# Optimization experiments

Hardware: AMD Instinct MI355X
Metric: run time of the kernel (lower is better)

Reference implementation:

```python
import jax, jax.numpy as jnp
import numpy as np
from jax.scipy.special import logsumexp

B, L, WLEN = 8, 64, 32
VOCAB, EMB, HID, REC = 30000, 256, 512, 128
PRIOR_FACTOR = 1.0
NEG = -1e9


def setup_inputs():
    key = jax.random.key(0)
    ks = jax.random.split(key, 12)
    h2 = HID // 2
    s = lambda k, shape, sc=0.05: jax.random.normal(k, shape, jnp.float32) * sc
    return {
        "sents": jax.random.randint(ks[0], (B, L, WLEN), 0, VOCAB),
        "mask": jnp.ones((B, L, WLEN), jnp.float32),
        "prior": jax.random.normal(ks[1], (B, L, L), dtype=jnp.float32),
        "heads": jax.random.randint(ks[2], (B, L), 0, L),
        "emb": s(ks[3], (VOCAB, EMB), 0.1),
        "Wih_f": s(ks[4], (4 * h2, EMB)), "Whh_f": s(ks[5], (4 * h2, h2)),
        "bih_f": jnp.zeros((4 * h2,), jnp.float32), "bhh_f": jnp.zeros((4 * h2,), jnp.float32),
        "Wih_b": s(ks[6], (4 * h2, EMB)), "Whh_b": s(ks[7], (4 * h2, h2)),
        "bih_b": jnp.zeros((4 * h2,), jnp.float32), "bhh_b": jnp.zeros((4 * h2,), jnp.float32),
        "W1": s(ks[8], (REC, HID)), "b1": jnp.zeros((REC,), jnp.float32),
        "W2": s(ks[9], (REC, HID)), "b2": jnp.zeros((REC,), jnp.float32),
        "Ws": s(ks[10], (1, 6 * HID)), "bs": jnp.zeros((1,), jnp.float32),
    }


def _lstm_dir(x, Wih, Whh, bih, bhh, reverse):
    # torch nn.LSTM default (no batch_first) scans over dim0; we faithfully scan axis 0.
    Hh = Whh.shape[1]
    bias = bih + bhh

    def step(carry, xt):
        h, c = carry
        g = xt @ Wih.T + h @ Whh.T + bias  # [L, 4H], gate order i,f,g,o
        i, f, gg, o = jnp.split(g, 4, axis=-1)
        c = jax.nn.sigmoid(f) * c + jax.nn.sigmoid(i) * jnp.tanh(gg)
        h = jax.nn.sigmoid(o) * jnp.tanh(c)
        return (h, c), h

    z = jnp.zeros((x.shape[1], Hh), x.dtype)
    _, hs = jax.lax.scan(step, (z, z), x, reverse=reverse)
    return hs


def _eisner_log_partition(s):
    # Eisner inside algorithm (log partition over projective trees rooted at index 0).
    Bz, n = s.shape[0], s.shape[1]
    eye = jnp.eye(n, dtype=s.dtype)
    init = jnp.tile(jnp.where(eye > 0, 0.0, NEG)[None], (Bz, 1, 1))
    C_r, C_l = init, init
    I_r = jnp.full((Bz, n, n), NEG, s.dtype)
    I_l = I_r
    for w in range(1, n):  # static unroll over span widths (sequential DP)
        i = np.arange(n - w)
        j = i + w
        k0 = i[:, None] + np.arange(w)[None, :]         # k = i..j-1
        inc = logsumexp(C_r[:, i[:, None], k0] + C_l[:, k0 + 1, j[:, None]], axis=2)
        I_r = I_r.at[:, i, j].set(inc + s[:, i, j])
        I_l = I_l.at[:, i, j].set(inc + s[:, j, i])
        k1 = i[:, None] + np.arange(1, w + 1)[None, :]  # k = i+1..j
        C_r = C_r.at[:, i, j].set(logsumexp(I_r[:, i[:, None], k1] + C_r[:, k1, j[:, None]], axis=2))
        C_l = C_l.at[:, i, j].set(logsumexp(C_l[:, i[:, None], k0] + I_l[:, k0, j[:, None]], axis=2))
    return C_r[:, 0, n - 1]


def _forward(sents, mask, prior, heads, emb, Wih_f, Whh_f, bih_f, bhh_f,
             Wih_b, Whh_b, bih_b, bhh_b, W1, b1, W2, b2, Ws, bs):
    words = emb[sents]                                   # [B,L,W,E]
    elen = mask.sum(-1)                                  # [B,L]
    embeds = (words * mask[..., None]).sum(2) / (elen + (elen == 0))[..., None]
    h = jnp.concatenate([_lstm_dir(embeds, Wih_f, Whh_f, bih_f, bhh_f, False),
                         _lstm_dir(embeds, Wih_b, Whh_b, bih_b, bhh_b, True)], axis=-1)  # [B,L,HID]
    xn = jnp.pad(h[:, 1:], ((0, 0), (0, 1), (0, 0)))     # next-EDU shift
    xb = jnp.pad(h[:, :-1], ((0, 0), (1, 0), (0, 0)))    # prev-EDU shift
    trio = jnp.concatenate([h, xb, xn], axis=-1)         # [B,L,3*HID]
    Bz, n, F3 = trio.shape
    # pairwise feature tensor (materialized as in the original module)
    f = jnp.concatenate([jnp.broadcast_to(trio[:, :, None, :], (Bz, n, n, F3)),
                         jnp.broadcast_to(trio[:, None, :, :], (Bz, n, n, F3))], axis=-1)
    crf = jnp.einsum('bijk,k->bij', f, Ws[0]) + bs[0]    # [B,n,n]
    p1 = h @ W1.T + b1
    p2 = h @ W2.T + b2
    recons = jax.nn.log_softmax(jnp.einsum('bik,bjk->bij', p1, p2), axis=-1)
    jp = crf + recons + (PRIOR_FACTOR / n) * prior
    logZ = _eisner_log_partition(crf)                    # [B]
    g = jp[jnp.arange(Bz)[:, None], heads[:, 1:], jnp.arange(1, n)[None, :]]  # [B,n-1]
    best = logsumexp(g, axis=1)
    return -(best - logZ).mean()


def reference(sents, mask, prior, heads, emb, Wih_f, Whh_f, bih_f, bhh_f,
              Wih_b, Whh_b, bih_b, bhh_b, W1, b1, W2, b2, Ws, bs):
    return _forward(sents, mask, prior, heads, emb, Wih_f, Whh_f, bih_f, bhh_f,
                    Wih_b, Whh_b, bih_b, bhh_b, W1, b1, W2, b2, Ws, bs)
```

## Files before the change

### kernel.cpp

```cpp
#include <hip/hip_runtime.h>
#include <hip/hip_bf16.h>
#include <math.h>

#define L2E 1.44269504f
#define LN2 0.69314718f
#define TSTRIDE 68

typedef __attribute__((ext_vector_type(2))) float floatx2;

__device__ __forceinline__ float sigf(float x){ return 1.0f/(1.0f+expf(-x)); }

__device__ __forceinline__ float quad_max(float x) {
    x = fmaxf(x, __int_as_float(__builtin_amdgcn_mov_dpp(__float_as_int(x), 0xB1, 0xF, 0xF, true)));
    x = fmaxf(x, __int_as_float(__builtin_amdgcn_mov_dpp(__float_as_int(x), 0x4E, 0xF, 0xF, true)));
    return x;
}
__device__ __forceinline__ float oct_sum(float x) {
    x += __int_as_float(__builtin_amdgcn_mov_dpp(__float_as_int(x), 0xB1, 0xF, 0xF, true));
    x += __int_as_float(__builtin_amdgcn_mov_dpp(__float_as_int(x), 0x4E, 0xF, 0xF, true));
    x += __int_as_float(__builtin_amdgcn_mov_dpp(__float_as_int(x), 0x141, 0xF, 0xF, true));
    return x;
}

__global__ __launch_bounds__(256) void prep_all(const float* __restrict__ Whh_f, const float* __restrict__ Whh_b,
                             const float* __restrict__ bih_f, const float* __restrict__ bhh_f,
                             const float* __restrict__ bih_b, const float* __restrict__ bhh_b,
                             uint4* __restrict__ qWf, uint4* __restrict__ qWb,
                             float* __restrict__ scf, float* __restrict__ scb,
                             float* __restrict__ biasf, float* __restrict__ biasb,
                             const int* __restrict__ sents, const float* __restrict__ mask,
                             const float* __restrict__ emb, float* __restrict__ embeds,
                             float* __restrict__ out) {
    int tid = threadIdx.x;
    if (blockIdx.x < 512) {
        int bl = blockIdx.x;
        const int*   srow = sents + bl*32;
        const float* mrow = mask  + bl*32;
        float acc = 0.0f, el = 0.0f;
        for (int w = 0; w < 32; ++w) {
            float m = mrow[w];
            el  += m;
            acc += emb[(size_t)srow[w]*256 + tid] * m;
        }
        float den = el + (el == 0.0f ? 1.0f : 0.0f);
        embeds[bl*256 + tid] = acc / den;
        if (bl == 0)      { for (int q = tid; q < 1024; q += 256) biasf[q] = bih_f[q] + bhh_f[q]; }
        else if (bl == 1) { for (int q = tid; q < 1024; q += 256) biasb[q] = bih_b[q] + bhh_b[q]; }
        else if (bl == 2 && tid == 0) out[0] = 0.0f;
    } else {
        int pb  = blockIdx.x - 512;
        int dir = pb >> 6;
        int cg  = pb & 63;
        const float* W = dir ? Whh_b : Whh_f;
        uint4* qW = dir ? qWb : qWf;
        float* sc = dir ? scb : scf;
        __shared__ float Wl[16][260];
        __shared__ float sL[16];
        #pragma unroll
        for (int lr = 0; lr < 16; ++lr) {
            int g = lr >> 2, jj = lr & 3;
            int rowid = g*256 + cg*4 + jj;
            Wl[lr][tid] = W[(size_t)rowid*256 + tid];
        }
        __syncthreads();
        if (tid < 64) {
            int lr = tid >> 2, sub = tid & 3;
            float mx = 0.0f;
            for (int m = 0; m < 64; ++m) mx = fmaxf(mx, fabsf(Wl[lr][sub*64 + m]));
            mx = quad_max(mx);
            if (sub == 0) sL[lr] = mx * (1.0f/240.0f) + 1e-30f;
        }
        __syncthreads();
        int k4 = tid >> 2, jj = tid & 3;
        float is0 = 1.0f / sL[0*4 + jj];
        float is1 = 1.0f / sL[1*4 + jj];
        float is2 = 1.0f / sL[2*4 + jj];
        float is3 = 1.0f / sL[3*4 + jj];
        uint4 q;
        unsigned int* qq = (unsigned int*)&q;
        #pragma unroll
        for (int kk = 0; kk < 4; ++kk) {
            int k = k4*4 + kk;
            int d = 0;
            d = __builtin_amdgcn_cvt_pk_fp8_f32(Wl[0*4+jj][k]*is0, Wl[1*4+jj][k]*is1, d, false);
            d = __builtin_amdgcn_cvt_pk_fp8_f32(Wl[2*4+jj][k]*is2, Wl[3*4+jj][k]*is3, d, true);
            qq[kk] = (unsigned int)d;
        }
        qW[k4*256 + cg*4 + jj] = q;
        if (tid < 16) {
            int g = tid >> 2, j2 = tid & 3;
            sc[(cg*4 + j2)*4 + g] = sL[g*4 + j2];
        }
    }
}

__device__ __forceinline__ void gemm64_body(const float* __restrict__ A,
                                            const float* __restrict__ Bm,
                                            const float* __restrict__ bias,
                                            float* __restrict__ C,
                                            int N, int K, int bx, int by) {
    __shared__ __align__(16) float As[32][68];
    __shared__ __align__(16) float Bs[32][68];
    int tid = threadIdx.x;
    int tx = tid & 15, ty = tid >> 4;
    int row0 = bx * 64, col0 = by * 64;
    float acc[4][4];
    #pragma unroll
    for (int r = 0; r < 4; ++r)
        #pragma unroll
        for (int c = 0; c < 4; ++c) acc[r][c] = 0.0f;
    int lr = tid >> 2;
    int lc = (tid & 3) * 8;
    for (int k0 = 0; k0 < K; k0 += 32) {
        float4 a0 = *(const float4*)(A  + (size_t)(row0+lr)*K + k0 + lc);
        float4 a1 = *(const float4*)(A  + (size_t)(row0+lr)*K + k0 + lc + 4);
        float4 b0 = *(const float4*)(Bm + (size_t)(col0+lr)*K + k0 + lc);
        float4 b1 = *(const float4*)(Bm + (size_t)(col0+lr)*K + k0 + lc + 4);
        As[lc  ][lr] = a0.x; As[lc+1][lr] = a0.y; As[lc+2][lr] = a0.z; As[lc+3][lr] = a0.w;
        As[lc+4][lr] = a1.x; As[lc+5][lr] = a1.y; As[lc+6][lr] = a1.z; As[lc+7][lr] = a1.w;
        Bs[lc  ][lr] = b0.x; Bs[lc+1][lr] = b0.y; Bs[lc+2][lr] = b0.z; Bs[lc+3][lr] = b0.w;
        Bs[lc+4][lr] = b1.x; Bs[lc+5][lr] = b1.y; Bs[lc+6][lr] = b1.z; Bs[lc+7][lr] = b1.w;
        __syncthreads();
        #pragma unroll
        for (int kc = 0; kc < 32; ++kc) {
            float4 xa = *(const float4*)&As[kc][ty*4];
            float4 xb = *(const float4*)&Bs[kc][tx*4];
            acc[0][0] = fmaf(xa.x, xb.x, acc[0][0]);
            acc[0][1] = fmaf(xa.x, xb.y, acc[0][1]);
            acc[0][2] = fmaf(xa.x, xb.z, acc[0][2]);
            acc[0][3] = fmaf(xa.x, xb.w, acc[0][3]);
            acc[1][0] = fmaf(xa.y, xb.x, acc[1][0]);
            acc[1][1] = fmaf(xa.y, xb.y, acc[1][1]);
            acc[1][2] = fmaf(xa.y, xb.z, acc[1][2]);
            acc[1][3] = fmaf(xa.y, xb.w, acc[1][3]);
            acc[2][0] = fmaf(xa.z, xb.x, acc[2][0]);
            acc[2][1] = fmaf(xa.z, xb.y, acc[2][1]);
            acc[2][2] = fmaf(xa.z, xb.z, acc[2][2]);
            acc[2][3] = fmaf(xa.z, xb.w, acc[2][3]);
            acc[3][0] = fmaf(xa.w, xb.x, acc[3][0]);
            acc[3][1] = fmaf(xa.w, xb.y, acc[3][1]);
            acc[3][2] = fmaf(xa.w, xb.z, acc[3][2]);
            acc[3][3] = fmaf(xa.w, xb.w, acc[3][3]);
        }
        __syncthreads();
    }
    float4 bv = bias ? *(const float4*)&bias[col0 + tx*4] : make_float4(0.f,0.f,0.f,0.f);
    #pragma unroll
    for (int r = 0; r < 4; ++r) {
        float4 o;
        o.x = acc[r][0] + bv.x; o.y = acc[r][1] + bv.y;
        o.z = acc[r][2] + bv.z; o.w = acc[r][3] + bv.w;
        *(float4*)(C + (size_t)(row0 + ty*4 + r)*N + col0 + tx*4) = o;
    }
}

__device__ __forceinline__ void gemm32_body(const float* __restrict__ A,
                                            const float* __restrict__ Bm,
                                            const float* __restrict__ bias,
                                            float* __restrict__ C,
                                            int N, int K, int bx, int by) {
    __shared__ __align__(16) float As[32][36];
    __shared__ __align__(16) float Bs[32][36];
    int tid = threadIdx.x;
    int tx = tid & 15, ty = tid >> 4;
    int row0 = bx * 32, col0 = by * 32;
    float acc00 = 0.f, acc01 = 0.f, acc10 = 0.f, acc11 = 0.f;
    int lr = tid >> 3;
    int lc = (tid & 7) * 4;
    for (int k0 = 0; k0 < K; k0 += 32) {
        float4 a0 = *(const float4*)(A  + (size_t)(row0+lr)*K + k0 + lc);
        float4 b0 = *(const float4*)(Bm + (size_t)(col0+lr)*K + k0 + lc);
        As[lc  ][lr] = a0.x; As[lc+1][lr] = a0.y; As[lc+2][lr] = a0.z; As[lc+3][lr] = a0.w;
        Bs[lc  ][lr] = b0.x; Bs[lc+1][lr] = b0.y; Bs[lc+2][lr] = b0.z; Bs[lc+3][lr] = b0.w;
        __syncthreads();
        #pragma unroll
        for (int kc = 0; kc < 32; ++kc) {
            float2 xa = *(const float2*)&As[kc][ty*2];
            float2 xb = *(const float2*)&Bs[kc][tx*2];
            acc00 = fmaf(xa.x, xb.x, acc00);
            acc01 = fmaf(xa.x, xb.y, acc01);
            acc10 = fmaf(xa.y, xb.x, acc10);
            acc11 = fmaf(xa.y, xb.y, acc11);
        }
        __syncthreads();
    }
    float2 bv = *(const float2*)&bias[col0 + tx*2];
    float2 o0; o0.x = acc00 + bv.x; o0.y = acc01 + bv.y;
    float2 o1; o1.x = acc10 + bv.x; o1.y = acc11 + bv.y;
    *(float2*)(C + (size_t)(row0 + ty*2    )*N + col0 + tx*2) = o0;
    *(float2*)(C + (size_t)(row0 + ty*2 + 1)*N + col0 + tx*2) = o1;
}

__global__ __launch_bounds__(256) void gemm_ih(const float* __restrict__ embeds,
                                               const float* __restrict__ Wf, const float* __restrict__ Wb,
                                               const float* __restrict__ biasf, const float* __restrict__ biasb,
                                               float* __restrict__ gxf, float* __restrict__ gxb) {
    int dir = blockIdx.z;
    gemm64_body(embeds, dir ? Wb : Wf, dir ? biasb : biasf, dir ? gxb : gxf,
                1024, 256, blockIdx.x, blockIdx.y);
}

__global__ __launch_bounds__(512) void lstm_rec(const float* __restrict__ gxf,
                                                const float* __restrict__ gxb,
                                                const uint4* __restrict__ qWf,
                                                const uint4* __restrict__ qWb,
                                                const float* __restrict__ scf,
                                                const float* __restrict__ scb,
                                                float* __restrict__ hall) {
    int blk  = blockIdx.x;
    int rep  = blk >> 7;
    blk &= 127;
    int dir  = blk >> 6;
    int pos  = blk & 63;
    int tid  = threadIdx.x;
    int j    = tid & 255;
    int half = tid >> 8;
    const float* gx = dir ? gxb : gxf;
    const uint4* qW = dir ? qWb : qWf;
    float4 sc = ((const float4*)(dir ? scb : scf))[j];
    __shared__ __align__(16) float hs[256];
    __shared__ __align__(16) float part[256][4];
    if (tid < 256) hs[tid] = 0.0f;
    float cellc = 0.0f;
    __syncthreads();
    const uint4* qWh = qW + (half << 13);
    const float* hsh = hs + (half << 7);
    for (int s = 0; s < 8; ++s) {
        int t = dir ? (7 - s) : s;
        const float* g0 = gx + (size_t)(t*64 + pos)*1024;
        float ai = 0.0f, af = 0.0f, ag = 0.0f, ao = 0.0f;
        if (half == 0) { ai = g0[j]; af = g0[256+j]; ag = g0[512+j]; ao = g0[768+j]; }
        float qi = 0.0f, qf = 0.0f, qg = 0.0f, qo = 0.0f;
        #pragma unroll 8
        for (int k4 = 0; k4 < 32; ++k4) {
            uint4 wq = qWh[(k4 << 8) + j];
            float4 hp = *(const float4*)&hsh[k4*4];
            floatx2 pa, pb;
            pa = __builtin_amdgcn_cvt_pk_f32_fp8(wq.x, false);
            pb = __builtin_amdgcn_cvt_pk_f32_fp8(wq.x, true);
            qi = fmaf(pa.x, hp.x, qi); qf = fmaf(pa.y, hp.x, qf);
            qg = fmaf(pb.x, hp.x, qg); qo = fmaf(pb.y, hp.x, qo);
            pa = __builtin_amdgcn_cvt_pk_f32_fp8(wq.y, false);
            pb = __builtin_amdgcn_cvt_pk_f32_fp8(wq.y, true);
            qi = fmaf(pa.x, hp.y, qi); qf = fmaf(pa.y, hp.y, qf);
            qg = fmaf(pb.x, hp.y, qg); qo = fmaf(pb.y, hp.y, qo);
            pa = __builtin_amdgcn_cvt_pk_f32_fp8(wq.z, false);
            pb = __builtin_amdgcn_cvt_pk_f32_fp8(wq.z, true);
            qi = fmaf(pa.x, hp.z, qi); qf = fmaf(pa.y, hp.z, qf);
            qg = fmaf(pb.x, hp.z, qg); qo = fmaf(pb.y, hp.z, qo);
            pa = __builtin_amdgcn_cvt_pk_f32_fp8(wq.w, false);
            pb = __builtin_amdgcn_cvt_pk_f32_fp8(wq.w, true);
            qi = fmaf(pa.x, hp.w, qi); qf = fmaf(pa.y, hp.w, qf);
            qg = fmaf(pb.x, hp.w, qg); qo = fmaf(pb.y, hp.w, qo);
        }
        if (half) { part[j][0] = qi; part[j][1] = qf; part[j][2] = qg; part[j][3] = qo; }
        __syncthreads();
        if (half == 0) {
            float4 pr = *(const float4*)&part[j][0];
            ai = fmaf(sc.x, qi + pr.x, ai);
            af = fmaf(sc.y, qf + pr.y, af);
            ag = fmaf(sc.z, qg + pr.z, ag);
            ao = fmaf(sc.w, qo + pr.w, ao);
            cellc = sigf(af)*cellc + sigf(ai)*tanhf(ag);
            float h0 = sigf(ao)*tanhf(cellc);
            hs[j] = h0;
            if (rep == 0) hall[(size_t)(t*64 + pos)*512 + dir*256 + j] = h0;
        }
        __syncthreads();
    }
}

__global__ __launch_bounds__(256) void post_lstm(const float* __restrict__ hall,
                                                 const float* __restrict__ Ws,
                                                 float* __restrict__ u, float* __restrict__ v,
                                                 const float* __restrict__ W1, const float* __restrict__ b1,
                                                 const float* __restrict__ W2, const float* __restrict__ b2,
                                                 float* __restrict__ p1, float* __restrict__ p2) {
    if (blockIdx.x < 512) {
        int bi = blockIdx.x;
        int i  = bi & 63;
        int tid = threadIdx.x;
        float pu = 0.0f, pv = 0.0f;
        for (int q = tid; q < 1536; q += 256) {
            int seg = q >> 9, kk = q & 511;
            float tv = 0.0f;
            if (seg == 0)       tv = hall[(size_t)bi*512 + kk];
            else if (seg == 1)  { if (i > 0)  tv = hall[(size_t)(bi-1)*512 + kk]; }
            else                { if (i < 63) tv = hall[(size_t)(bi+1)*512 + kk]; }
            pu = fmaf(tv, Ws[q],        pu);
            pv = fmaf(tv, Ws[1536 + q], pv);
        }
        for (int off = 32; off; off >>= 1) { pu += __shfl_xor(pu, off); pv += __shfl_xor(pv, off); }
        __shared__ float ru[4], rv[4];
        int wv = tid >> 6, lane = tid & 63;
        if (lane == 0) { ru[wv] = pu; rv[wv] = pv; }
        __syncthreads();
        if (tid == 0) { u[bi] = ru[0]+ru[1]+ru[2]+ru[3]; v[bi] = rv[0]+rv[1]+rv[2]+rv[3]; }
    } else {
        int gb = blockIdx.x - 512;
        int sel = gb >> 6; gb &= 63;
        gemm32_body(hall, sel ? W2 : W1, sel ? b2 : b1, sel ? p2 : p1,
                    128, 512, gb >> 2, gb & 3);
    }
}

__global__ __launch_bounds__(512, 2) void eisner_final(const float* __restrict__ u,
                                                    const float* __restrict__ v,
                                                    const float* __restrict__ bs,
                                                    const float* __restrict__ p1,
                                                    const float* __restrict__ p2,
                                                    const float* __restrict__ prior,
                                                    const int* __restrict__ heads,
                                                    float* __restrict__ out) {
    int b   = blockIdx.x & 7;
    int rep = blockIdx.x >> 3;
    __shared__ __align__(16) float SMEM[3*64*TSTRIDE + 64];
    __shared__ float su[64], sv[64], lseSb[64], sBest[1];
    float* T1 = &SMEM[0];
    float* T2 = &SMEM[64*TSTRIDE];
    float* T3 = &SMEM[2*64*TSTRIDE];
    int tid = threadIdx.x;
    float bsv = bs[0];
    if (tid < 64) {
        su[tid] = u[b*64 + tid];
        sv[tid] = v[b*64 + tid];
    }
    const float4* g1 = (const float4*)(p1 + (size_t)b*8192);
    const float4* g2 = (const float4*)(p2 + (size_t)b*8192);
    float4* s1p = (float4*)SMEM;
    float4* s2p = (float4*)(SMEM + 64*TSTRIDE);
    int r   = tid >> 3;
    int sub = tid & 7;
    float acc[8];
    #pragma unroll
    for (int q = 0; q < 8; ++q) acc[q] = 0.0f;
    for (int p = 0; p < 2; ++p) {
        #pragma unroll
        for (int f0 = 0; f0 < 4; ++f0) {
            int f = f0*512 + tid;
            int half = f >> 10;
            int ff = f & 1023;
            int row = ff >> 4, c4 = ff & 15;
            float4 vv = (half ? g2 : g1)[row*32 + (p<<4) + c4];
            (half ? s2p : s1p)[row*17 + c4] = vv;
        }
        __syncthreads();
        #pragma unroll 2
        for (int k4 = 0; k4 < 16; ++k4) {
            float4 a = s1p[r*17 + k4];
            #pragma unroll
            for (int q = 0; q < 8; ++q) {
                float4 bv = s2p[(sub + (q<<3))*17 + k4];
                acc[q] = fmaf(a.x, bv.x, acc[q]);
                acc[q] = fmaf(a.y, bv.y, acc[q]);
                acc[q] = fmaf(a.z, bv.z, acc[q]);
                acc[q] = fmaf(a.w, bv.w, acc[q]);
            }
        }
        __syncthreads();
    }
    float pm = acc[0];
    #pragma unroll
    for (int q = 1; q < 8; ++q) pm = fmaxf(pm, acc[q]);
    pm = fmaxf(pm, __int_as_float(__builtin_amdgcn_mov_dpp(__float_as_int(pm), 0xB1, 0xF, 0xF, true)));
    pm = fmaxf(pm, __int_as_float(__builtin_amdgcn_mov_dpp(__float_as_int(pm), 0x4E, 0xF, 0xF, true)));
    pm = fmaxf(pm, __int_as_float(__builtin_amdgcn_mov_dpp(__float_as_int(pm), 0x141, 0xF, 0xF, true)));
    float ps = 0.0f;
    #pragma unroll
    for (int q = 0; q < 8; ++q) ps += exp2f((acc[q] - pm) * L2E);
    ps = oct_sum(ps);
    if (sub == 0) lseSb[r] = pm + log2f(ps) * LN2;
    float* Sl = SMEM;
    #pragma unroll
    for (int q = 0; q < 8; ++q) Sl[r*66 + sub + (q<<3)] = acc[q];
    __syncthreads();
    if (tid < 64) {
        int m = tid;
        float gv = -INFINITY;
        if (m >= 1) {
            int hd = heads[b*64 + m];
            gv = su[hd] + sv[m] + bsv + (Sl[hd*66 + m] - lseSb[hd])
               + prior[(size_t)(b*64 + hd)*64 + m] * (1.0f/64.0f);
        }
        float mm = gv;
        for (int off = 32; off; off >>= 1) mm = fmaxf(mm, __shfl_xor(mm, off));
        float se = (m >= 1) ? exp2f((gv - mm) * L2E) : 0.0f;
        for (int off = 32; off; off >>= 1) se += __shfl_xor(se, off);
        if (m == 0) sBest[0] = mm + log2f(se) * LN2;
    }
    __syncthreads();
    for (int q = tid; q < 3*64*TSTRIDE; q += 512) SMEM[q] = 0.0f;
    __syncthreads();
    if (tid < 64) {
        T1[tid*TSTRIDE + tid] = 1.0f;
        if (tid >= 1) T2[tid*TSTRIDE + tid-1] = 1.0f;
    }
    __syncthreads();
    int i = r;
    int k0 = i & ~3;
    float sui_b = su[i] + bsv;
    float svi_b = sv[i] + bsv;
    const float* t1i = &T1[i*TSTRIDE];
    const float* t2i = &T2[i*TSTRIDE];
    const float* t3i = &T3[i*TSTRIDE];
    for (int w = 1; w < 64; ++w) {
        int ns = 64 - w;
        if (i < ns) {
            int j = i + w;
            const float* t1j = &T1[j*TSTRIDE];
            const float* t2j = &T2[j*TSTRIDE];
            const float* t3j = &T3[j*TSTRIDE];
            float eDr = exp2f((sui_b + sv[j]) * L2E);
            float eDl = exp2f((su[j] + svi_b) * L2E);
            float s1 = 0.0f, sr = 0.0f, sl = 0.0f;
            #pragma unroll
            for (int t = 0; t < 2; ++t) {
                int k = k0 + ((t << 3) + sub) * 4;
                if (k < j) {
                    float4 a1  = *(const float4*)&t1i[k];
                    float4 b1  = *(const float4*)&t2j[k];
                    float4 a2  = *(const float4*)&t3i[k];
                    float4 b2v = *(const float4*)&t1j[k];
                    float4 a3  = *(const float4*)&t2i[k];
                    float4 b3  = *(const float4*)&t3j[k];
                    #pragma unroll
                    for (int c = 0; c < 4; ++c) {
                        s1 = fmaf(((const float*)&a1)[c], ((const float*)&b1)[c],  s1);
                        sr = fmaf(((const float*)&a2)[c], ((const float*)&b2v)[c], sr);
                        sl = fmaf(((const float*)&a3)[c], ((const float*)&b3)[c],  sl);
                    }
                }
            }
            s1 = oct_sum(s1);
            sr = oct_sum(sr);
            sl = oct_sum(sl);
            if (sub == 0) {
                float Ir = 0.25f * s1 * eDr;
                float Il = 0.25f * s1 * eDl;
                float Cr = sr + Ir;
                float Cl = sl + Il;
                T3[i*TSTRIDE + j] = Ir;
                T1[i*TSTRIDE + j] = Cr;
                T1[j*TSTRIDE + i] = Cr;
                T3[j*TSTRIDE + i] = Il;
                T2[i*TSTRIDE + j] = Cl;
                if (i >= 1) T2[j*TSTRIDE + i-1] = Cl;
            }
        }
        __syncthreads();
    }
    if (rep == 0 && tid == 0) {
        float logZv = (log2f(T1[0*TSTRIDE + 63]) + 126.0f) * LN2;
        atomicAdd(out, -(sBest[0] - logZv) * 0.125f);
    }
}

extern "C" void kernel_launch(void* const* d_in, const int* in_sizes, int n_in,
                              void* d_out, int out_size, void* d_ws, size_t ws_size,
                              hipStream_t stream) {
    const int*   sents = (const int*)  d_in[0];
    const float* mask  = (const float*)d_in[1];
    const float* prior = (const float*)d_in[2];
    const int*   heads = (const int*)  d_in[3];
    const float* emb   = (const float*)d_in[4];
    const float* Wih_f = (const float*)d_in[5];
    const float* Whh_f = (const float*)d_in[6];
    const float* bih_f = (const float*)d_in[7];
    const float* bhh_f = (const float*)d_in[8];
    const float* Wih_b = (const float*)d_in[9];
    const float* Whh_b = (const float*)d_in[10];
    const float* bih_b = (const float*)d_in[11];
    const float* bhh_b = (const float*)d_in[12];
    const float* W1    = (const float*)d_in[13];
    const float* b1    = (const float*)d_in[14];
    const float* W2    = (const float*)d_in[15];
    const float* b2    = (const float*)d_in[16];
    const float* Ws    = (const float*)d_in[17];
    const float* bs    = (const float*)d_in[18];
    float* out = (float*)d_out;

    char* w = (char*)d_ws;
    float* embeds = (float*)(w + 0);
    float* gxf    = (float*)(w + 524288);
    float* gxb    = (float*)(w + 2621440);
    uint4* qWf    = (uint4*)(w + 4718592);
    uint4* qWb    = (uint4*)(w + 4980736);
    float* scf    = (float*)(w + 5242880);
    float* scb    = (float*)(w + 5246976);
    float* biasf  = (float*)(w + 5767168);
    float* biasb  = (float*)(w + 5771264);
    float* hall   = (float*)(w + 5775360);
    float* uArr   = (float*)(w + 6823936);
    float* vArr   = (float*)(w + 6825984);
    float* p1     = (float*)(w + 6828032);
    float* p2     = (float*)(w + 7090176);

    prep_all<<<640, 256, 0, stream>>>(Whh_f, Whh_b, bih_f, bhh_f, bih_b, bhh_b,
                                      qWf, qWb, scf, scb, biasf, biasb,
                                      sents, mask, emb, embeds, out);
    gemm_ih<<<dim3(8,16,2), 256, 0, stream>>>(embeds, Wih_f, Wih_b, biasf, biasb, gxf, gxb);
    lstm_rec<<<256, 512, 0, stream>>>(gxf, gxb, qWf, qWb, scf, scb, hall);
    post_lstm<<<640, 256, 0, stream>>>(hall, Ws, uArr, vArr, W1, b1, W2, b2, p1, p2);
    eisner_final<<<256, 512, 0, stream>>>(uArr, vArr, bs, p1, p2, prior, heads, out);
    (void)in_sizes; (void)n_in; (void)out_size; (void)ws_size;
}
```

Before: 208.9 us.

## Fuse GEMM, LSTM, post-LSTM and Eisner stages into one persistent kernel with grid barriers

Merges the four kernels that ran after prep (input GEMM, LSTM recurrence, post-LSTM projections, Eisner DP) into one persistent kernel of 256 blocks. The stages are separated by a software grid barrier built on an atomic counter, which prep_all resets. The aim is to remove kernel launch gaps and tail effects between stages. The risks are deadlock if all 256 blocks of 512 threads are not co-resident, plus atomic spin overhead, and several stages now have their work split differently across blocks.

```diff
diff --git a/kernel.cpp b/kernel.cpp
--- a/kernel.cpp
+++ b/kernel.cpp
@@ -13,6 +13,12 @@
 __device__ __forceinline__ float quad_max(float x) {
     x = fmaxf(x, __int_as_float(__builtin_amdgcn_mov_dpp(__float_as_int(x), 0xB1, 0xF, 0xF, true)));
     x = fmaxf(x, __int_as_float(__builtin_amdgcn_mov_dpp(__float_as_int(x), 0x4E, 0xF, 0xF, true)));
+    return x;
+}
+__device__ __forceinline__ float oct_max(float x) {
+    x = fmaxf(x, __int_as_float(__builtin_amdgcn_mov_dpp(__float_as_int(x), 0xB1, 0xF, 0xF, true)));
+    x = fmaxf(x, __int_as_float(__builtin_amdgcn_mov_dpp(__float_as_int(x), 0x4E, 0xF, 0xF, true)));
+    x = fmaxf(x, __int_as_float(__builtin_amdgcn_mov_dpp(__float_as_int(x), 0x141, 0xF, 0xF, true)));
     return x;
 }
 __device__ __forceinline__ float oct_sum(float x) {
@@ -20,6 +26,17 @@
     x += __int_as_float(__builtin_amdgcn_mov_dpp(__float_as_int(x), 0x4E, 0xF, 0xF, true));
     x += __int_as_float(__builtin_amdgcn_mov_dpp(__float_as_int(x), 0x141, 0xF, 0xF, true));
     return x;
+}
+
+__device__ __forceinline__ void gbar(unsigned* cnt, unsigned target) {
+    __threadfence();
+    __syncthreads();
+    if (threadIdx.x == 0) {
+        atomicAdd(cnt, 1u);
+        while (atomicAdd(cnt, 0u) < target) __builtin_amdgcn_s_sleep(10);
+    }
+    __syncthreads();
+    __threadfence();
 }
 
 __global__ __launch_bounds__(256) void prep_all(const float* __restrict__ Whh_f, const float* __restrict__ Whh_b,
@@ -30,7 +47,7 @@
                              float* __restrict__ biasf, float* __restrict__ biasb,
                              const int* __restrict__ sents, const float* __restrict__ mask,
                              const float* __restrict__ emb, float* __restrict__ embeds,
-                             float* __restrict__ out) {
+                             float* __restrict__ out, unsigned* __restrict__ bar) {
     int tid = threadIdx.x;
     if (blockIdx.x < 512) {
         int bl = blockIdx.x;
@@ -46,7 +63,7 @@
         embeds[bl*256 + tid] = acc / den;
         if (bl == 0)      { for (int q = tid; q < 1024; q += 256) biasf[q] = bih_f[q] + bhh_f[q]; }
         else if (bl == 1) { for (int q = tid; q < 1024; q += 256) biasb[q] = bih_b[q] + bhh_b[q]; }
-        else if (bl == 2 && tid == 0) out[0] = 0.0f;
+        else if (bl == 2 && tid == 0) { out[0] = 0.0f; atomicExch(bar, 0u); }
     } else {
         int pb  = blockIdx.x - 512;
         int dir = pb >> 6;
@@ -94,364 +111,357 @@
     }
 }
 
-__device__ __forceinline__ void gemm64_body(const float* __restrict__ A,
-                                            const float* __restrict__ Bm,
-                                            const float* __restrict__ bias,
-                                            float* __restrict__ C,
-                                            int N, int K, int bx, int by) {
-    __shared__ __align__(16) float As[32][68];
-    __shared__ __align__(16) float Bs[32][68];
-    int tid = threadIdx.x;
-    int tx = tid & 15, ty = tid >> 4;
-    int row0 = bx * 64, col0 = by * 64;
-    float acc[4][4];
-    #pragma unroll
-    for (int r = 0; r < 4; ++r)
-        #pragma unroll
-        for (int c = 0; c < 4; ++c) acc[r][c] = 0.0f;
-    int lr = tid >> 2;
-    int lc = (tid & 3) * 8;
-    for (int k0 = 0; k0 < K; k0 += 32) {
-        float4 a0 = *(const float4*)(A  + (size_t)(row0+lr)*K + k0 + lc);
-        float4 a1 = *(const float4*)(A  + (size_t)(row0+lr)*K + k0 + lc + 4);
-        float4 b0 = *(const float4*)(Bm + (size_t)(col0+lr)*K + k0 + lc);
-        float4 b1 = *(const float4*)(Bm + (size_t)(col0+lr)*K + k0 + lc + 4);
-        As[lc  ][lr] = a0.x; As[lc+1][lr] = a0.y; As[lc+2][lr] = a0.z; As[lc+3][lr] = a0.w;
-        As[lc+4][lr] = a1.x; As[lc+5][lr] = a1.y; As[lc+6][lr] = a1.z; As[lc+7][lr] = a1.w;
-        Bs[lc  ][lr] = b0.x; Bs[lc+1][lr] = b0.y; Bs[lc+2][lr] = b0.z; Bs[lc+3][lr] = b0.w;
-        Bs[lc+4][lr] = b1.x; Bs[lc+5][lr] = b1.y; Bs[lc+6][lr] = b1.z; Bs[lc+7][lr] = b1.w;
-        __syncthreads();
-        #pragma unroll
-        for (int kc = 0; kc < 32; ++kc) {
-            float4 xa = *(const float4*)&As[kc][ty*4];
-            float4 xb = *(const float4*)&Bs[kc][tx*4];
-            acc[0][0] = fmaf(xa.x, xb.x, acc[0][0]);
-            acc[0][1] = fmaf(xa.x, xb.y, acc[0][1]);
-            acc[0][2] = fmaf(xa.x, xb.z, acc[0][2]);
-            acc[0][3] = fmaf(xa.x, xb.w, acc[0][3]);
-            acc[1][0] = fmaf(xa.y, xb.x, acc[1][0]);
-            acc[1][1] = fmaf(xa.y, xb.y, acc[1][1]);
-            acc[1][2] = fmaf(xa.y, xb.z, acc[1][2]);
-            acc[1][3] = fmaf(xa.y, xb.w, acc[1][3]);
-            acc[2][0] = fmaf(xa.z, xb.x, acc[2][0]);
-            acc[2][1] = fmaf(xa.z, xb.y, acc[2][1]);
-            acc[2][2] = fmaf(xa.z, xb.z, acc[2][2]);
-            acc[2][3] = fmaf(xa.z, xb.w, acc[2][3]);
-            acc[3][0] = fmaf(xa.w, xb.x, acc[3][0]);
-            acc[3][1] = fmaf(xa.w, xb.y, acc[3][1]);
-            acc[3][2] = fmaf(xa.w, xb.z, acc[3][2]);
-            acc[3][3] = fmaf(xa.w, xb.w, acc[3][3]);
-        }
-        __syncthreads();
-    }
-    float4 bv = bias ? *(const float4*)&bias[col0 + tx*4] : make_float4(0.f,0.f,0.f,0.f);
-    #pragma unroll
-    for (int r = 0; r < 4; ++r) {
-        float4 o;
-        o.x = acc[r][0] + bv.x; o.y = acc[r][1] + bv.y;
-        o.z = acc[r][2] + bv.z; o.w = acc[r][3] + bv.w;
-        *(float4*)(C + (size_t)(row0 + ty*4 + r)*N + col0 + tx*4) = o;
-    }
-}
-
-__device__ __forceinline__ void gemm32_body(const float* __restrict__ A,
-                                            const float* __restrict__ Bm,
-                                            const float* __restrict__ bias,
-                                            float* __restrict__ C,
-                                            int N, int K, int bx, int by) {
-    __shared__ __align__(16) float As[32][36];
-    __shared__ __align__(16) float Bs[32][36];
-    int tid = threadIdx.x;
-    int tx = tid & 15, ty = tid >> 4;
-    int row0 = bx * 32, col0 = by * 32;
-    float acc00 = 0.f, acc01 = 0.f, acc10 = 0.f, acc11 = 0.f;
-    int lr = tid >> 3;
-    int lc = (tid & 7) * 4;
-    for (int k0 = 0; k0 < K; k0 += 32) {
-        float4 a0 = *(const float4*)(A  + (size_t)(row0+lr)*K + k0 + lc);
-        float4 b0 = *(const float4*)(Bm + (size_t)(col0+lr)*K + k0 + lc);
-        As[lc  ][lr] = a0.x; As[lc+1][lr] = a0.y; As[lc+2][lr] = a0.z; As[lc+3][lr] = a0.w;
-        Bs[lc  ][lr] = b0.x; Bs[lc+1][lr] = b0.y; Bs[lc+2][lr] = b0.z; Bs[lc+3][lr] = b0.w;
-        __syncthreads();
-        #pragma unroll
-        for (int kc = 0; kc < 32; ++kc) {
-            float2 xa = *(const float2*)&As[kc][ty*2];
-            float2 xb = *(const float2*)&Bs[kc][tx*2];
-            acc00 = fmaf(xa.x, xb.x, acc00);
-            acc01 = fmaf(xa.x, xb.y, acc01);
-            acc10 = fmaf(xa.y, xb.x, acc10);
-            acc11 = fmaf(xa.y, xb.y, acc11);
-        }
-        __syncthreads();
-    }
-    float2 bv = *(const float2*)&bias[col0 + tx*2];
-    float2 o0; o0.x = acc00 + bv.x; o0.y = acc01 + bv.y;
-    float2 o1; o1.x = acc10 + bv.x; o1.y = acc11 + bv.y;
-    *(float2*)(C + (size_t)(row0 + ty*2    )*N + col0 + tx*2) = o0;
-    *(float2*)(C + (size_t)(row0 + ty*2 + 1)*N + col0 + tx*2) = o1;
-}
-
-__global__ __launch_bounds__(256) void gemm_ih(const float* __restrict__ embeds,
-                                               const float* __restrict__ Wf, const float* __restrict__ Wb,
-                                               const float* __restrict__ biasf, const float* __restrict__ biasb,
-                                               float* __restrict__ gxf, float* __restrict__ gxb) {
-    int dir = blockIdx.z;
-    gemm64_body(embeds, dir ? Wb : Wf, dir ? biasb : biasf, dir ? gxb : gxf,
-                1024, 256, blockIdx.x, blockIdx.y);
-}
-
-__global__ __launch_bounds__(512) void lstm_rec(const float* __restrict__ gxf,
-                                                const float* __restrict__ gxb,
-                                                const uint4* __restrict__ qWf,
-                                                const uint4* __restrict__ qWb,
-                                                const float* __restrict__ scf,
-                                                const float* __restrict__ scb,
-                                                float* __restrict__ hall) {
-    int blk  = blockIdx.x;
-    int rep  = blk >> 7;
-    blk &= 127;
-    int dir  = blk >> 6;
-    int pos  = blk & 63;
-    int tid  = threadIdx.x;
-    int j    = tid & 255;
-    int half = tid >> 8;
-    const float* gx = dir ? gxb : gxf;
-    const uint4* qW = dir ? qWb : qWf;
-    float4 sc = ((const float4*)(dir ? scb : scf))[j];
-    __shared__ __align__(16) float hs[256];
-    __shared__ __align__(16) float part[256][4];
-    if (tid < 256) hs[tid] = 0.0f;
-    float cellc = 0.0f;
-    __syncthreads();
-    const uint4* qWh = qW + (half << 13);
-    const float* hsh = hs + (half << 7);
-    for (int s = 0; s < 8; ++s) {
-        int t = dir ? (7 - s) : s;
-        const float* g0 = gx + (size_t)(t*64 + pos)*1024;
-        float ai = 0.0f, af = 0.0f, ag = 0.0f, ao = 0.0f;
-        if (half == 0) { ai = g0[j]; af = g0[256+j]; ag = g0[512+j]; ao = g0[768+j]; }
-        float qi = 0.0f, qf = 0.0f, qg = 0.0f, qo = 0.0f;
-        #pragma unroll 8
-        for (int k4 = 0; k4 < 32; ++k4) {
-            uint4 wq = qWh[(k4 << 8) + j];
-            float4 hp = *(const float4*)&hsh[k4*4];
-            floatx2 pa, pb;
-            pa = __builtin_amdgcn_cvt_pk_f32_fp8(wq.x, false);
-            pb = __builtin_amdgcn_cvt_pk_f32_fp8(wq.x, true);
-            qi = fmaf(pa.x, hp.x, qi); qf = fmaf(pa.y, hp.x, qf);
-            qg = fmaf(pb.x, hp.x, qg); qo = fmaf(pb.y, hp.x, qo);
-            pa = __builtin_amdgcn_cvt_pk_f32_fp8(wq.y, false);
-            pb = __builtin_amdgcn_cvt_pk_f32_fp8(wq.y, true);
-            qi = fmaf(pa.x, hp.y, qi); qf = fmaf(pa.y, hp.y, qf);
-            qg = fmaf(pb.x, hp.y, qg); qo = fmaf(pb.y, hp.y, qo);
-            pa = __builtin_amdgcn_cvt_pk_f32_fp8(wq.z, false);
-            pb = __builtin_amdgcn_cvt_pk_f32_fp8(wq.z, true);
-            qi = fmaf(pa.x, hp.z, qi); qf = fmaf(pa.y, hp.z, qf);
-            qg = fmaf(pb.x, hp.z, qg); qo = fmaf(pb.y, hp.z, qo);
-            pa = __builtin_amdgcn_cvt_pk_f32_fp8(wq.w, false);
-            pb = __builtin_amdgcn_cvt_pk_f32_fp8(wq.w, true);
-            qi = fmaf(pa.x, hp.w, qi); qf = fmaf(pa.y, hp.w, qf);
-            qg = fmaf(pb.x, hp.w, qg); qo = fmaf(pb.y, hp.w, qo);
-        }
-        if (half) { part[j][0] = qi; part[j][1] = qf; part[j][2] = qg; part[j][3] = qo; }
-        __syncthreads();
-        if (half == 0) {
-            float4 pr = *(const float4*)&part[j][0];
-            ai = fmaf(sc.x, qi + pr.x, ai);
-            af = fmaf(sc.y, qf + pr.y, af);
-            ag = fmaf(sc.z, qg + pr.z, ag);
-            ao = fmaf(sc.w, qo + pr.w, ao);
-            cellc = sigf(af)*cellc + sigf(ai)*tanhf(ag);
-            float h0 = sigf(ao)*tanhf(cellc);
-            hs[j] = h0;
-            if (rep == 0) hall[(size_t)(t*64 + pos)*512 + dir*256 + j] = h0;
-        }
-        __syncthreads();
-    }
-}
-
-__global__ __launch_bounds__(256) void post_lstm(const float* __restrict__ hall,
-                                                 const float* __restrict__ Ws,
-                                                 float* __restrict__ u, float* __restrict__ v,
-                                                 const float* __restrict__ W1, const float* __restrict__ b1,
-                                                 const float* __restrict__ W2, const float* __restrict__ b2,
-                                                 float* __restrict__ p1, float* __restrict__ p2) {
-    if (blockIdx.x < 512) {
-        int bi = blockIdx.x;
-        int i  = bi & 63;
-        int tid = threadIdx.x;
-        float pu = 0.0f, pv = 0.0f;
-        for (int q = tid; q < 1536; q += 256) {
-            int seg = q >> 9, kk = q & 511;
-            float tv = 0.0f;
-            if (seg == 0)       tv = hall[(size_t)bi*512 + kk];
-            else if (seg == 1)  { if (i > 0)  tv = hall[(size_t)(bi-1)*512 + kk]; }
-            else                { if (i < 63) tv = hall[(size_t)(bi+1)*512 + kk]; }
-            pu = fmaf(tv, Ws[q],        pu);
-            pv = fmaf(tv, Ws[1536 + q], pv);
-        }
-        for (int off = 32; off; off >>= 1) { pu += __shfl_xor(pu, off); pv += __shfl_xor(pv, off); }
-        __shared__ float ru[4], rv[4];
-        int wv = tid >> 6, lane = tid & 63;
-        if (lane == 0) { ru[wv] = pu; rv[wv] = pv; }
-        __syncthreads();
-        if (tid == 0) { u[bi] = ru[0]+ru[1]+ru[2]+ru[3]; v[bi] = rv[0]+rv[1]+rv[2]+rv[3]; }
-    } else {
-        int gb = blockIdx.x - 512;
-        int sel = gb >> 6; gb &= 63;
-        gemm32_body(hall, sel ? W2 : W1, sel ? b2 : b1, sel ? p2 : p1,
-                    128, 512, gb >> 2, gb & 3);
-    }
-}
-
-__global__ __launch_bounds__(512, 2) void eisner_final(const float* __restrict__ u,
-                                                    const float* __restrict__ v,
-                                                    const float* __restrict__ bs,
-                                                    const float* __restrict__ p1,
-                                                    const float* __restrict__ p2,
-                                                    const float* __restrict__ prior,
-                                                    const int* __restrict__ heads,
-                                                    float* __restrict__ out) {
-    int b   = blockIdx.x & 7;
-    int rep = blockIdx.x >> 3;
+__global__ __launch_bounds__(512, 2) void fused_main(
+        const float* __restrict__ embeds,
+        const float* __restrict__ Wih_f, const float* __restrict__ Wih_b,
+        const float* __restrict__ biasf, const float* __restrict__ biasb,
+        float* __restrict__ gxf, float* __restrict__ gxb,
+        const uint4* __restrict__ qWf, const uint4* __restrict__ qWb,
+        const float* __restrict__ scf, const float* __restrict__ scb,
+        float* __restrict__ hall,
+        const float* __restrict__ Ws, float* __restrict__ u, float* __restrict__ v,
+        const float* __restrict__ W1, const float* __restrict__ b1,
+        const float* __restrict__ W2, const float* __restrict__ b2,
+        float* __restrict__ p1, float* __restrict__ p2,
+        const float* __restrict__ bs, const float* __restrict__ prior,
+        const int* __restrict__ heads,
+        float* __restrict__ out, unsigned* __restrict__ bar) {
     __shared__ __align__(16) float SMEM[3*64*TSTRIDE + 64];
     __shared__ float su[64], sv[64], lseSb[64], sBest[1];
-    float* T1 = &SMEM[0];
-    float* T2 = &SMEM[64*TSTRIDE];
-    float* T3 = &SMEM[2*64*TSTRIDE];
+    __shared__ float ru2[2][4], rv2[2][4];
     int tid = threadIdx.x;
-    float bsv = bs[0];
-    if (tid < 64) {
-        su[tid] = u[b*64 + tid];
-        sv[tid] = v[b*64 + tid];
+    int blk = blockIdx.x;
+
+    {
+        int dir  = blk >> 7;
+        int rest = blk & 127;
+        int bx = rest >> 4, by = rest & 15;
+        const float* A    = embeds;
+        const float* Bm   = dir ? Wih_b : Wih_f;
+        const float* bias = dir ? biasb : biasf;
+        float* C          = dir ? gxb : gxf;
+        const int N = 1024, K = 256;
+        float* As = SMEM;
+        float* Bs = SMEM + 32*68;
+        int tx = tid & 15, ty = tid >> 4;
+        int row0 = bx * 64, col0 = by * 64;
+        float acc[2][4];
+        #pragma unroll
+        for (int r = 0; r < 2; ++r)
+            #pragma unroll
+            for (int c = 0; c < 4; ++c) acc[r][c] = 0.0f;
+        int lr = tid >> 3;
+        int lc = (tid & 7) * 4;
+        for (int k0 = 0; k0 < K; k0 += 32) {
+            float4 a0 = *(const float4*)(A  + (size_t)(row0+lr)*K + k0 + lc);
+            float4 b0 = *(const float4*)(Bm + (size_t)(col0+lr)*K + k0 + lc);
+            As[(lc  )*68 + lr] = a0.x; As[(lc+1)*68 + lr] = a0.y;
+            As[(lc+2)*68 + lr] = a0.z; As[(lc+3)*68 + lr] = a0.w;
+            Bs[(lc  )*68 + lr] = b0.x; Bs[(lc+1)*68 + lr] = b0.y;
+            Bs[(lc+2)*68 + lr] = b0.z; Bs[(lc+3)*68 + lr] = b0.w;
+            __syncthreads();
+            #pragma unroll
+            for (int kc = 0; kc < 32; ++kc) {
+                float2 xa = *(const float2*)&As[kc*68 + ty*2];
+                float4 xb = *(const float4*)&Bs[kc*68 + tx*4];
+                acc[0][0] = fmaf(xa.x, xb.x, acc[0][0]);
+                acc[0][1] = fmaf(xa.x, xb.y, acc[0][1]);
+                acc[0][2] = fmaf(xa.x, xb.z, acc[0][2]);
+                acc[0][3] = fmaf(xa.x, xb.w, acc[0][3]);
+                acc[1][0] = fmaf(xa.y, xb.x, acc[1][0]);
+                acc[1][1] = fmaf(xa.y, xb.y, acc[1][1]);
+                acc[1][2] = fmaf(xa.y, xb.z, acc[1][2]);
+                acc[1][3] = fmaf(xa.y, xb.w, acc[1][3]);
+            }
+            __syncthreads();
+        }
+        float4 bv = *(const float4*)&bias[col0 + tx*4];
+        #pragma unroll
+        for (int r = 0; r < 2; ++r) {
+            float4 o;
+            o.x = acc[r][0] + bv.x; o.y = acc[r][1] + bv.y;
+            o.z = acc[r][2] + bv.z; o.w = acc[r][3] + bv.w;
+            *(float4*)(C + (size_t)(row0 + ty*2 + r)*N + col0 + tx*4) = o;
+        }
     }
-    const float4* g1 = (const float4*)(p1 + (size_t)b*8192);
-    const float4* g2 = (const float4*)(p2 + (size_t)b*8192);
-    float4* s1p = (float4*)SMEM;
-    float4* s2p = (float4*)(SMEM + 64*TSTRIDE);
-    int r   = tid >> 3;
-    int sub = tid & 7;
-    float acc[8];
-    #pragma unroll
-    for (int q = 0; q < 8; ++q) acc[q] = 0.0f;
-    for (int p = 0; p < 2; ++p) {
-        #pragma unroll
-        for (int f0 = 0; f0 < 4; ++f0) {
-            int f = f0*512 + tid;
-            int half = f >> 10;
-            int ff = f & 1023;
-            int row = ff >> 4, c4 = ff & 15;
-            float4 vv = (half ? g2 : g1)[row*32 + (p<<4) + c4];
-            (half ? s2p : s1p)[row*17 + c4] = vv;
-        }
-        __syncthreads();
-        #pragma unroll 2
-        for (int k4 = 0; k4 < 16; ++k4) {
-            float4 a = s1p[r*17 + k4];
+    gbar(bar, 256);
+
+    {
+        int lb   = blk;
+        int rep  = lb >> 7;
+        lb &= 127;
+        int dir  = lb >> 6;
+        int pos  = lb & 63;
+        int j    = tid & 255;
+        int half = tid >> 8;
+        const float* gx = dir ? gxb : gxf;
+        const uint4* qW = dir ? qWb : qWf;
+        float4 sc = ((const float4*)(dir ? scb : scf))[j];
+        float* hs = SMEM;
+        float (*part)[4] = (float(*)[4])(SMEM + 256);
+        if (tid < 256) hs[tid] = 0.0f;
+        float cellc = 0.0f;
+        __syncthreads();
+        const uint4* qWh = qW + (half << 13);
+        const float* hsh = hs + (half << 7);
+        for (int s = 0; s < 8; ++s) {
+            int t = dir ? (7 - s) : s;
+            const float* g0 = gx + (size_t)(t*64 + pos)*1024;
+            float ai = 0.0f, af = 0.0f, ag = 0.0f, ao = 0.0f;
+            if (half == 0) { ai = g0[j]; af = g0[256+j]; ag = g0[512+j]; ao = g0[768+j]; }
+            float qi = 0.0f, qf = 0.0f, qg = 0.0f, qo = 0.0f;
+            #pragma unroll 8
+            for (int k4 = 0; k4 < 32; ++k4) {
+                uint4 wq = qWh[(k4 << 8) + j];
+                float4 hp = *(const float4*)&hsh[k4*4];
+                floatx2 pa, pb;
+                pa = __builtin_amdgcn_cvt_pk_f32_fp8(wq.x, false);
+                pb = __builtin_amdgcn_cvt_pk_f32_fp8(wq.x, true);
+                qi = fmaf(pa.x, hp.x, qi); qf = fmaf(pa.y, hp.x, qf);
+                qg = fmaf(pb.x, hp.x, qg); qo = fmaf(pb.y, hp.x, qo);
+                pa = __builtin_amdgcn_cvt_pk_f32_fp8(wq.y, false);
+                pb = __builtin_amdgcn_cvt_pk_f32_fp8(wq.y, true);
+                qi = fmaf(pa.x, hp.y, qi); qf = fmaf(pa.y, hp.y, qf);
+                qg = fmaf(pb.x, hp.y, qg); qo = fmaf(pb.y, hp.y, qo);
+                pa = __builtin_amdgcn_cvt_pk_f32_fp8(wq.z, false);
+                pb = __builtin_amdgcn_cvt_pk_f32_fp8(wq.z, true);
+                qi = fmaf(pa.x, hp.z, qi); qf = fmaf(pa.y, hp.z, qf);
+                qg = fmaf(pb.x, hp.z, qg); qo = fmaf(pb.y, hp.z, qo);
+                pa = __builtin_amdgcn_cvt_pk_f32_fp8(wq.w, false);
+                pb = __builtin_amdgcn_cvt_pk_f32_fp8(wq.w, true);
+                qi = fmaf(pa.x, hp.w, qi); qf = fmaf(pa.y, hp.w, qf);
+                qg = fmaf(pb.x, hp.w, qg); qo = fmaf(pb.y, hp.w, qo);
+            }
+            if (half) { part[j][0] = qi; part[j][1] = qf; part[j][2] = qg; part[j][3] = qo; }
+            __syncthreads();
+            if (half == 0) {
+                float4 pr = *(const float4*)&part[j][0];
+                ai = fmaf(sc.x, qi + pr.x, ai);
+                af = fmaf(sc.y, qf + pr.y, af);
+                ag = fmaf(sc.z, qg + pr.z, ag);
+                ao = fmaf(sc.w, qo + pr.w, ao);
+                cellc = sigf(af)*cellc + sigf(ai)*tanhf(ag);
+                float h0 = sigf(ao)*tanhf(cellc);
+                hs[j] = h0;
+                if (rep == 0) hall[(size_t)(t*64 + pos)*512 + dir*256 + j] = h0;
+            }
+            __syncthreads();
+        }
+    }
+    gbar(bar, 512);
+
+    if (blk >= 128) {
+        int h  = tid >> 8;
+        int t2 = tid & 255;
+        for (int p = 0; p < 2; ++p) {
+            int bi = (blk - 128)*4 + p*2 + h;
+            int i  = bi & 63;
+            float pu = 0.0f, pv = 0.0f;
+            for (int q = t2; q < 1536; q += 256) {
+                int seg = q >> 9, kk = q & 511;
+                float tv = 0.0f;
+                if (seg == 0)       tv = hall[(size_t)bi*512 + kk];
+                else if (seg == 1)  { if (i > 0)  tv = hall[(size_t)(bi-1)*512 + kk]; }
+                else                { if (i < 63) tv = hall[(size_t)(bi+1)*512 + kk]; }
+                pu = fmaf(tv, Ws[q],        pu);
+                pv = fmaf(tv, Ws[1536 + q], pv);
+            }
+            for (int off = 32; off; off >>= 1) { pu += __shfl_xor(pu, off); pv += __shfl_xor(pv, off); }
+            int wv = t2 >> 6, lane = t2 & 63;
+            if (lane == 0) { ru2[h][wv] = pu; rv2[h][wv] = pv; }
+            __syncthreads();
+            if (t2 == 0) {
+                u[bi] = ru2[h][0]+ru2[h][1]+ru2[h][2]+ru2[h][3];
+                v[bi] = rv2[h][0]+rv2[h][1]+rv2[h][2]+rv2[h][3];
+            }
+            __syncthreads();
+        }
+    } else {
+        int sel = blk >> 6, un = blk & 63;
+        const float* A    = hall;
+        const float* Bm   = sel ? W2 : W1;
+        const float* bias = sel ? b2 : b1;
+        float* C          = sel ? p2 : p1;
+        int bx = un >> 2, by = un & 3;
+        const int N = 128, K = 512;
+        float* As2 = SMEM;
+        float* Bs2 = SMEM + 32*36;
+        int tx = tid & 15, ty = (tid >> 4) & 15;
+        int row0 = bx * 32, col0 = by * 32;
+        float a00 = 0.f, a01 = 0.f, a10 = 0.f, a11 = 0.f;
+        int lr = (tid >> 3) & 31;
+        int lc = (tid & 7) * 4;
+        for (int k0 = 0; k0 < K; k0 += 32) {
+            if (tid < 256) {
+                float4 av = *(const float4*)(A  + (size_t)(row0+lr)*K + k0 + lc);
+                float4 bv = *(const float4*)(Bm + (size_t)(col0+lr)*K + k0 + lc);
+                As2[(lc  )*36 + lr] = av.x; As2[(lc+1)*36 + lr] = av.y;
+                As2[(lc+2)*36 + lr] = av.z; As2[(lc+3)*36 + lr] = av.w;
+                Bs2[(lc  )*36 + lr] = bv.x; Bs2[(lc+1)*36 + lr] = bv.y;
+                Bs2[(lc+2)*36 + lr] = bv.z; Bs2[(lc+3)*36 + lr] = bv.w;
+            }
+            __syncthreads();
+            if (tid < 256) {
+                #pragma unroll
+                for (int kc = 0; kc < 32; ++kc) {
+                    float2 xa = *(const float2*)&As2[kc*36 + ty*2];
+                    float2 xb = *(const float2*)&Bs2[kc*36 + tx*2];
+                    a00 = fmaf(xa.x, xb.x, a00);
+                    a01 = fmaf(xa.x, xb.y, a01);
+                    a10 = fmaf(xa.y, xb.x, a10);
+                    a11 = fmaf(xa.y, xb.y, a11);
+                }
+            }
+            __syncthreads();
+        }
+        if (tid < 256) {
+            float2 bv = *(const float2*)&bias[col0 + tx*2];
+            float2 o0; o0.x = a00 + bv.x; o0.y = a01 + bv.y;
+            float2 o1; o1.x = a10 + bv.x; o1.y = a11 + bv.y;
+            *(float2*)(C + (size_t)(row0 + ty*2    )*N + col0 + tx*2) = o0;
+            *(float2*)(C + (size_t)(row0 + ty*2 + 1)*N + col0 + tx*2) = o1;
+        }
+    }
+    gbar(bar, 768);
+
+    {
+        int b   = blk & 7;
+        int rep = blk >> 3;
+        float* T1 = &SMEM[0];
+        float* T2 = &SMEM[64*TSTRIDE];
+        float* T3 = &SMEM[2*64*TSTRIDE];
+        float bsv = bs[0];
+        if (tid < 64) {
+            su[tid] = u[b*64 + tid];
+            sv[tid] = v[b*64 + tid];
+        }
+        const float4* g1 = (const float4*)(p1 + (size_t)b*8192);
+        const float4* g2 = (const float4*)(p2 + (size_t)b*8192);
+        float4* s1p = (float4*)SMEM;
+        float4* s2p = (float4*)(SMEM + 64*TSTRIDE);
+        int r   = tid >> 3;
+        int sub = tid & 7;
+        float acc[8];
+        #pragma unroll
+        for (int q = 0; q < 8; ++q) acc[q] = 0.0f;
+        __syncthreads();
+        for (int p = 0; p < 2; ++p) {
             #pragma unroll
-            for (int q = 0; q < 8; ++q) {
-                float4 bv = s2p[(sub + (q<<3))*17 + k4];
-                acc[q] = fmaf(a.x, bv.x, acc[q]);
-                acc[q] = fmaf(a.y, bv.y, acc[q]);
-                acc[q] = fmaf(a.z, bv.z, acc[q]);
-                acc[q] = fmaf(a.w, bv.w, acc[q]);
-            }
-        }
-        __syncthreads();
-    }
-    float pm = acc[0];
-    #pragma unroll
-    for (int q = 1; q < 8; ++q) pm = fmaxf(pm, acc[q]);
-    pm = fmaxf(pm, __int_as_float(__builtin_amdgcn_mov_dpp(__float_as_int(pm), 0xB1, 0xF, 0xF, true)));
-    pm = fmaxf(pm, __int_as_float(__builtin_amdgcn_mov_dpp(__float_as_int(pm), 0x4E, 0xF, 0xF, true)));
-    pm = fmaxf(pm, __int_as_float(__builtin_amdgcn_mov_dpp(__float_as_int(pm), 0x141, 0xF, 0xF, true)));
-    float ps = 0.0f;
-    #pragma unroll
-    for (int q = 0; q < 8; ++q) ps += exp2f((acc[q] - pm) * L2E);
-    ps = oct_sum(ps);
-    if (sub == 0) lseSb[r] = pm + log2f(ps) * LN2;
-    float* Sl = SMEM;
-    #pragma unroll
-    for (int q = 0; q < 8; ++q) Sl[r*66 + sub + (q<<3)] = acc[q];
-    __syncthreads();
-    if (tid < 64) {
-        int m = tid;
-        float gv = -INFINITY;
-        if (m >= 1) {
-            int hd = heads[b*64 + m];
-            gv = su[hd] + sv[m] + bsv + (Sl[hd*66 + m] - lseSb[hd])
-               + prior[(size_t)(b*64 + hd)*64 + m] * (1.0f/64.0f);
-        }
-        float mm = gv;
-        for (int off = 32; off; off >>= 1) mm = fmaxf(mm, __shfl_xor(mm, off));
-        float se = (m >= 1) ? exp2f((gv - mm) * L2E) : 0.0f;
-        for (int off = 32; off; off >>= 1) se += __shfl_xor(se, off);
-        if (m == 0) sBest[0] = mm + log2f(se) * LN2;
-    }
-    __syncthreads();
-    for (int q = tid; q < 3*64*TSTRIDE; q += 512) SMEM[q] = 0.0f;
-    __syncthreads();
-    if (tid < 64) {
-        T1[tid*TSTRIDE + tid] = 1.0f;
-        if (tid >= 1) T2[tid*TSTRIDE + tid-1] = 1.0f;
-    }
-    __syncthreads();
-    int i = r;
-    int k0 = i & ~3;
-    float sui_b = su[i] + bsv;
-    float svi_b = sv[i] + bsv;
-    const float* t1i = &T1[i*TSTRIDE];
-    const float* t2i = &T2[i*TSTRIDE];
-    const float* t3i = &T3[i*TSTRIDE];
-    for (int w = 1; w < 64; ++w) {
-        int ns = 64 - w;
-        if (i < ns) {
-            int j = i + w;
-            const float* t1j = &T1[j*TSTRIDE];
-            const float* t2j = &T2[j*TSTRIDE];
-            const float* t3j = &T3[j*TSTRIDE];
-            float eDr = exp2f((sui_b + sv[j]) * L2E);
-            float eDl = exp2f((su[j] + svi_b) * L2E);
-            float s1 = 0.0f, sr = 0.0f, sl = 0.0f;
-            #pragma unroll
-            for (int t = 0; t < 2; ++t) {
-                int k = k0 + ((t << 3) + sub) * 4;
-                if (k < j) {
-                    float4 a1  = *(const float4*)&t1i[k];
-                    float4 b1  = *(const float4*)&t2j[k];
-                    float4 a2  = *(const float4*)&t3i[k];
-                    float4 b2v = *(const float4*)&t1j[k];
-                    float4 a3  = *(const float4*)&t2i[k];
-                    float4 b3  = *(const float4*)&t3j[k];
-                    #pragma unroll
-                    for (int c = 0; c < 4; ++c) {
-                        s1 = fmaf(((const float*)&a1)[c], ((const float*)&b1)[c],  s1);
-                        sr = fmaf(((const float*)&a2)[c], ((const float*)&b2v)[c], sr);
-                        sl = fmaf(((const float*)&a3)[c], ((const float*)&b3)[c],  sl);
+            for (int f0 = 0; f0 < 4; ++f0) {
+                int f = f0*512 + tid;
+                int half = f >> 10;
+                int ff = f & 1023;
+                int row = ff >> 4, c4 = ff & 15;
+                float4 vv = (half ? g2 : g1)[row*32 + (p<<4) + c4];
+                (half ? s2p : s1p)[row*17 + c4] = vv;
+            }
+            __syncthreads();
+            #pragma unroll 2
+            for (int k4 = 0; k4 < 16; ++k4) {
+                float4 a = s1p[r*17 + k4];
+                #pragma unroll
+                for (int q = 0; q < 8; ++q) {
+                    float4 bv = s2p[(sub + (q<<3))*17 + k4];
+                    acc[q] = fmaf(a.x, bv.x, acc[q]);
+                    acc[q] = fmaf(a.y, bv.y, acc[q]);
+                    acc[q] = fmaf(a.z, bv.z, acc[q]);
+                    acc[q] = fmaf(a.w, bv.w, acc[q]);
+                }
+            }
+            __syncthreads();
+        }
+        float pm = acc[0];
+        #pragma unroll
+        for (int q = 1; q < 8; ++q) pm = fmaxf(pm, acc[q]);
+        pm = oct_max(pm);
+        float ps = 0.0f;
+        #pragma unroll
+        for (int q = 0; q < 8; ++q) ps += exp2f((acc[q] - pm) * L2E);
+        ps = oct_sum(ps);
+        if (sub == 0) lseSb[r] = pm + log2f(ps) * LN2;
+        float* Sl = SMEM;
+        #pragma unroll
+        for (int q = 0; q < 8; ++q) Sl[r*66 + sub + (q<<3)] = acc[q];
+        __syncthreads();
+        if (tid < 64) {
+            int m = tid;
+            float gv = -INFINITY;
+            if (m >= 1) {
+                int hd = heads[b*64 + m];
+                gv = su[hd] + sv[m] + bsv + (Sl[hd*66 + m] - lseSb[hd])
+                   + prior[(size_t)(b*64 + hd)*64 + m] * (1.0f/64.0f);
+            }
+            float mm = gv;
+            for (int off = 32; off; off >>= 1) mm = fmaxf(mm, __shfl_xor(mm, off));
+            float se = (m >= 1) ? exp2f((gv - mm) * L2E) : 0.0f;
+            for (int off = 32; off; off >>= 1) se += __shfl_xor(se, off);
+            if (m == 0) sBest[0] = mm + log2f(se) * LN2;
+        }
+        __syncthreads();
+        for (int q = tid; q < 3*64*TSTRIDE; q += 512) SMEM[q] = 0.0f;
+        __syncthreads();
+        if (tid < 64) {
+            T1[tid*TSTRIDE + tid] = 1.0f;
+            if (tid >= 1) T2[tid*TSTRIDE + tid-1] = 1.0f;
+        }
+        __syncthreads();
+        int i = r;
+        int k0 = i & ~3;
+        float sui_b = su[i] + bsv;
+        float svi_b = sv[i] + bsv;
+        const float* t1i = &T1[i*TSTRIDE];
+        const float* t2i = &T2[i*TSTRIDE];
+        const float* t3i = &T3[i*TSTRIDE];
+        for (int w = 1; w < 64; ++w) {
+            int ns = 64 - w;
+            if (i < ns) {
+                int j = i + w;
+                const float* t1j = &T1[j*TSTRIDE];
+                const float* t2j = &T2[j*TSTRIDE];
+                const float* t3j = &T3[j*TSTRIDE];
+                float eDr = exp2f((sui_b + sv[j]) * L2E);
+                float eDl = exp2f((su[j] + svi_b) * L2E);
+                float s1 = 0.0f, sr = 0.0f, sl = 0.0f;
+                #pragma unroll
+                for (int t = 0; t < 2; ++t) {
+                    int k = k0 + ((t << 3) + sub) * 4;
+                    if (k < j) {
+                        float4 a1  = *(const float4*)&t1i[k];
+                        float4 b1  = *(const float4*)&t2j[k];
+                        float4 a2  = *(const float4*)&t3i[k];
+                        float4 b2v = *(const float4*)&t1j[k];
+                        float4 a3  = *(const float4*)&t2i[k];
+                        float4 b3  = *(const float4*)&t3j[k];
+                        #pragma unroll
+                        for (int c = 0; c < 4; ++c) {
+                            s1 = fmaf(((const float*)&a1)[c], ((const float*)&b1)[c],  s1);
+                            sr = fmaf(((const float*)&a2)[c], ((const float*)&b2v)[c], sr);
+                            sl = fmaf(((const float*)&a3)[c], ((const float*)&b3)[c],  sl);
+                        }
                     }
                 }
-            }
-            s1 = oct_sum(s1);
-            sr = oct_sum(sr);
-            sl = oct_sum(sl);
-            if (sub == 0) {
-                float Ir = 0.25f * s1 * eDr;
-                float Il = 0.25f * s1 * eDl;
-                float Cr = sr + Ir;
-                float Cl = sl + Il;
-                T3[i*TSTRIDE + j] = Ir;
-                T1[i*TSTRIDE + j] = Cr;
-                T1[j*TSTRIDE + i] = Cr;
-                T3[j*TSTRIDE + i] = Il;
-                T2[i*TSTRIDE + j] = Cl;
-                if (i >= 1) T2[j*TSTRIDE + i-1] = Cl;
-            }
-        }
-        __syncthreads();
-    }
-    if (rep == 0 && tid == 0) {
-        float logZv = (log2f(T1[0*TSTRIDE + 63]) + 126.0f) * LN2;
-        atomicAdd(out, -(sBest[0] - logZv) * 0.125f);
+                s1 = oct_sum(s1);
+                sr = oct_sum(sr);
+                sl = oct_sum(sl);
+                if (sub == 0) {
+                    float Ir = 0.25f * s1 * eDr;
+                    float Il = 0.25f * s1 * eDl;
+                    float Cr = sr + Ir;
+                    float Cl = sl + Il;
+                    T3[i*TSTRIDE + j] = Ir;
+                    T1[i*TSTRIDE + j] = Cr;
+                    T1[j*TSTRIDE + i] = Cr;
+                    T3[j*TSTRIDE + i] = Il;
+                    T2[i*TSTRIDE + j] = Cl;
+                    if (i >= 1) T2[j*TSTRIDE + i-1] = Cl;
+                }
+            }
+            __syncthreads();
+        }
+        if (rep == 0 && tid == 0) {
+            float logZv = (log2f(T1[0*TSTRIDE + 63]) + 126.0f) * LN2;
+            atomicAdd(out, -(sBest[0] - logZv) * 0.125f);
+        }
     }
 }
 
@@ -494,13 +504,14 @@
     float* vArr   = (float*)(w + 6825984);
     float* p1     = (float*)(w + 6828032);
     float* p2     = (float*)(w + 7090176);
+    unsigned* bar = (unsigned*)(w + 7352320);
 
     prep_all<<<640, 256, 0, stream>>>(Whh_f, Whh_b, bih_f, bhh_f, bih_b, bhh_b,
                                       qWf, qWb, scf, scb, biasf, biasb,
-                                      sents, mask, emb, embeds, out);
-    gemm_ih<<<dim3(8,16,2), 256, 0, stream>>>(embeds, Wih_f, Wih_b, biasf, biasb, gxf, gxb);
-    lstm_rec<<<256, 512, 0, stream>>>(gxf, gxb, qWf, qWb, scf, scb, hall);
-    post_lstm<<<640, 256, 0, stream>>>(hall, Ws, uArr, vArr, W1, b1, W2, b2, p1, p2);
-    eisner_final<<<256, 512, 0, stream>>>(uArr, vArr, bs, p1, p2, prior, heads, out);
+                                      sents, mask, emb, embeds, out, bar);
+    fused_main<<<256, 512, 0, stream>>>(embeds, Wih_f, Wih_b, biasf, biasb, gxf, gxb,
+                                        qWf, qWb, scf, scb, hall,
+                                        Ws, uArr, vArr, W1, b1, W2, b2, p1, p2,
+                                        bs, prior, heads, out, bar);
     (void)in_sizes; (void)n_in; (void)out_size; (void)ws_size;
 }
```

Measured after the change: 426.0 us. 2.04x slower.
